# Performance work log

Hardware: AMD Instinct MI355X
Metric: run time of the kernel (lower is better)

## Reference

```python
import jax, jax.numpy as jnp
import numpy as np

B, S, H = 32, 256, 128
K, C, DSUB, O = 8, 4096, 16, 6  # PQ subspaces, ncentroids=4096, subvector dim, bits/symbol


def setup_inputs() -> dict:
    key = jax.random.key(0)
    ks = jax.random.split(key, 8)
    return {
        "z": jax.random.normal(ks[0], (B, S, 3), jnp.float32),
        "W1": jax.random.normal(ks[1], (3, H), jnp.float32) * 0.3,
        "b1": jax.random.normal(ks[2], (H,), jnp.float32) * 0.1,
        "W2": jax.random.normal(ks[3], (H, H), jnp.float32) * 0.1,
        "b2": jax.random.normal(ks[4], (H,), jnp.float32) * 0.1,
        "centroids": jax.random.normal(ks[5], (K, C, DSUB), jnp.float32),
        "W3": jax.random.normal(ks[6], (H, O), jnp.float32) * 0.1,
        "b3": jax.random.normal(ks[7], (O,), jnp.float32) * 0.1,
    }


def reference(z, W1, b1, W2, b2, centroids, W3, b3):
    # Small demapper MLP (layers 1-2, exact dense math)
    h1 = jax.nn.relu(z @ W1 + b1)            # [B,S,H]
    h2 = jax.nn.relu(h1 @ W2 + b2)           # [B,S,H] == layer3in
    N = B * S
    x = h2.reshape(N, K, DSUB)               # split rows into K PQ subvectors
    # Encode: nearest centroid per subspace (||x-c||^2 argmin; ||x||^2 is constant per row)
    dots = jnp.einsum("nkd,kcd->nkc", x, centroids)      # [N,K,C]
    c_norm = jnp.sum(centroids * centroids, axis=-1)      # [K,C]
    codes = jnp.argmin(c_norm[None, :, :] - 2.0 * dots, axis=-1)  # [N,K] int
    # LUT: precomputed centroid @ W3 per subspace
    W3r = W3.reshape(K, DSUB, O)
    lut = jnp.einsum("kcd,kdo->kco", centroids, W3r)      # [K,C,O]
    # Approximate matmul: sum of LUT entries selected by codes
    approx = jnp.sum(lut[jnp.arange(K)[None, :], codes], axis=1)  # [N,O]
    llr = (approx + b3).reshape(B, S * O)                 # [B, n]
    return llr
```

## Files before the change

### kernel.cpp

```cpp
#include <hip/hip_runtime.h>
#include <hip/hip_fp16.h>
#include <stdint.h>

#define NROWS 8192
#define HDIM  128
#define KSUB  8
#define NC    4096
#define DSUB  16
#define OUTD  6

#define FB_TAU 6e-5f
#define DOTSCALE (-2.0f / 4096.0f)

typedef _Float16 f16x8 __attribute__((ext_vector_type(8)));
typedef float    f32x4 __attribute__((ext_vector_type(4)));

#define XK_OFF 0u
#define CN_OFF 4194304u
#define B1_OFF 4325376u
#define PK_OFF 6422528u

__global__ __launch_bounds__(256) void prep_kernel(
    const float* __restrict__ z, const float* __restrict__ W1, const float* __restrict__ b1,
    const float* __restrict__ W2, const float* __restrict__ b2,
    const float* __restrict__ ce,
    float* __restrict__ xk, float* __restrict__ cnorm, f16x8* __restrict__ B1S)
{
    __shared__ float h1s[16 * HDIM];
    __shared__ float w2s[HDIM * 64];
    const int t = threadIdx.x;
    const int half = blockIdx.x >> 9;
    const int row0 = (blockIdx.x & 511) * 16;

    if (blockIdx.x < 512) {
        const int e = blockIdx.x * 256 + t;
        const int k    = e >> 14;
        const int tile = (e >> 6) & 255;
        const int lane = e & 63;
        const int col  = lane & 15;
        const int quad = lane >> 4;
        const int dims = (quad & 1) * 8;
        const int part = quad >> 1;
        const int n = tile * 16 + col;
        const float* cp = &ce[((size_t)k * NC + n) * DSUB + dims];
        f16x8 hi, lo;
        #pragma unroll
        for (int j = 0; j < 8; ++j) {
            const float s = cp[j] * 16.0f;
            const _Float16 h = (_Float16)s;
            hi[j] = h;
            lo[j] = (_Float16)(s - (float)h);
        }
        B1S[e] = part ? lo : hi;
    }

    if (blockIdx.x < (KSUB * NC) / 256) {
        const int g = blockIdx.x * 256 + t;
        const float4* cp = (const float4*)&ce[(size_t)g * DSUB];
        float nn = 0.f;
        #pragma unroll
        for (int q = 0; q < 4; ++q) {
            const float4 v = cp[q];
            nn = fmaf(v.x, v.x, nn); nn = fmaf(v.y, v.y, nn);
            nn = fmaf(v.z, v.z, nn); nn = fmaf(v.w, v.w, nn);
        }
        cnorm[g] = nn;
    }

    {
        const float4* g4 = (const float4*)W2;
        float4* s4 = (float4*)w2s;
        #pragma unroll
        for (int q = 0; q < 8; ++q) {
            const int idx = t + q * 256;
            const int k  = idx >> 4;
            const int cg = idx & 15;
            s4[k * 16 + cg] = g4[k * 32 + half * 16 + cg];
        }
    }

    #pragma unroll
    for (int e = 0; e < 8; ++e) {
        const int idx = e * 256 + t;
        const int r = idx >> 7, j = idx & 127;
        const int n = row0 + r;
        float acc = b1[j];
        acc = fmaf(z[n * 3 + 0], W1[0 * HDIM + j], acc);
        acc = fmaf(z[n * 3 + 1], W1[1 * HDIM + j], acc);
        acc = fmaf(z[n * 3 + 2], W1[2 * HDIM + j], acc);
        h1s[idx] = fmaxf(acc, 0.f);
    }
    __syncthreads();

    const int c2 = (t & 31) * 2;
    const int r2 = (t >> 5) * 2;
    float acc[2][2];
    acc[0][0] = acc[0][1] = acc[1][0] = acc[1][1] = 0.f;

    for (int k4 = 0; k4 < HDIM; k4 += 4) {
        float hh[2][4], ww[4][2];
        #pragma unroll
        for (int q = 0; q < 2; ++q) {
            const float4 v = *(const float4*)&h1s[(r2 + q) * HDIM + k4];
            hh[q][0] = v.x; hh[q][1] = v.y; hh[q][2] = v.z; hh[q][3] = v.w;
        }
        #pragma unroll
        for (int p = 0; p < 4; ++p) {
            const float2 v = *(const float2*)&w2s[(k4 + p) * 64 + c2];
            ww[p][0] = v.x; ww[p][1] = v.y;
        }
        #pragma unroll
        for (int q = 0; q < 2; ++q)
            #pragma unroll
            for (int p = 0; p < 4; ++p) {
                acc[q][0] = fmaf(hh[q][p], ww[p][0], acc[q][0]);
                acc[q][1] = fmaf(hh[q][p], ww[p][1], acc[q][1]);
            }
    }

    const int col0 = half * 64 + c2;
    const float2 bb = *(const float2*)&b2[col0];
    const int kk = col0 >> 4;
    const int dd = col0 & 15;
    #pragma unroll
    for (int q = 0; q < 2; ++q) {
        float2 o;
        o.x = fmaxf(acc[q][0] + bb.x, 0.f);
        o.y = fmaxf(acc[q][1] + bb.y, 0.f);
        *(float2*)&xk[((size_t)kk * NROWS + (row0 + r2 + q)) * DSUB + dd] = o;
    }
}

__global__ __launch_bounds__(256, 8) void argmin_kernel(
    const float* __restrict__ xk, const f16x8* __restrict__ B1S,
    const float* __restrict__ cnorm, unsigned long long* __restrict__ pk)
{
    __shared__ f16x8 cs[8 * 64];
    __shared__ float cnL[1024];
    const int t = threadIdx.x;
    const int lane = t & 63;
    const int wid  = t >> 6;
    const int k  = blockIdx.y;
    const int cz = blockIdx.z;
    const int rb = blockIdx.x * 4 + wid;
    const int col  = lane & 15;
    const int quad = lane >> 4;
    const int dims = (quad & 1) * 8;
    const int part = quad >> 1;

    {
        const float* cnp0 = &cnorm[k * NC + cz * 1024];
        #pragma unroll
        for (int q = 0; q < 4; ++q) cnL[t + q * 256] = cnp0[t + q * 256];
    }

    f16x8 A[2], A2[2];
    #pragma unroll
    for (int g = 0; g < 2; ++g) {
        const int row = rb * 32 + g * 16 + col;
        const float* xp = &xk[((size_t)k * NROWS + row) * DSUB + dims];
        f16x8 hi, lo;
        #pragma unroll
        for (int j = 0; j < 8; ++j) {
            const float s = xp[j] * 256.0f;
            const _Float16 h = (_Float16)s;
            hi[j] = h;
            lo[j] = (_Float16)(s - (float)h);
        }
        A[g]  = part ? lo : hi;
        A2[g] = part ? hi : lo;
    }

    float m1[2][4], m2[2][4];
    int   idx[2][4];
    #pragma unroll
    for (int g = 0; g < 2; ++g)
        #pragma unroll
        for (int j = 0; j < 4; ++j) { m1[g][j] = 1e30f; m2[g][j] = 1e30f; idx[g][j] = 0; }

    const f16x8* gp = &B1S[((size_t)k * 256 + cz * 64) * 64];

    for (int ch = 0; ch < 8; ++ch) {
        __syncthreads();
        {
            const uint4* g4 = (const uint4*)(gp + (size_t)ch * 512);
            uint4* s4 = (uint4*)cs;
            #pragma unroll
            for (int q = 0; q < 2; ++q) s4[t + q * 256] = g4[t + q * 256];
        }
        __syncthreads();

        #pragma unroll 2
        for (int tt = 0; tt < 8; ++tt) {
            const f16x8 b1 = cs[tt * 64 + lane];
            const float nrm = cnL[(ch * 8 + tt) * 16 + col];
            const f32x4 zz = {0.f, 0.f, 0.f, 0.f};
            f32x4 p0 = __builtin_amdgcn_mfma_f32_16x16x32_f16(A[0],  b1, zz, 0, 0, 0);
            p0       = __builtin_amdgcn_mfma_f32_16x16x32_f16(A2[0], b1, p0, 0, 0, 0);
            f32x4 p1 = __builtin_amdgcn_mfma_f32_16x16x32_f16(A[1],  b1, zz, 0, 0, 0);
            p1       = __builtin_amdgcn_mfma_f32_16x16x32_f16(A2[1], b1, p1, 0, 0, 0);
            const int c = ((cz * 64 + ch * 8 + tt) << 4) + col;
            #pragma unroll
            for (int j = 0; j < 4; ++j) {
                {
                    const float s = fmaf(p0[j], DOTSCALE, nrm);
                    const bool lt = s < m1[0][j];
                    m2[0][j] = __builtin_amdgcn_fmed3f(s, m1[0][j], m2[0][j]);
                    idx[0][j] = lt ? c : idx[0][j];
                    m1[0][j] = fminf(s, m1[0][j]);
                }
                {
                    const float s = fmaf(p1[j], DOTSCALE, nrm);
                    const bool lt = s < m1[1][j];
                    m2[1][j] = __builtin_amdgcn_fmed3f(s, m1[1][j], m2[1][j]);
                    idx[1][j] = lt ? c : idx[1][j];
                    m1[1][j] = fminf(s, m1[1][j]);
                }
            }
        }
    }

    #pragma unroll
    for (int off = 1; off < 16; off <<= 1) {
        #pragma unroll
        for (int g = 0; g < 2; ++g)
            #pragma unroll
            for (int j = 0; j < 4; ++j) {
                const float om1 = __shfl_xor(m1[g][j], off, 64);
                const float om2 = __shfl_xor(m2[g][j], off, 64);
                const int  oidx = __shfl_xor(idx[g][j], off, 64);
                const bool better = (om1 < m1[g][j]) ||
                                    (om1 == m1[g][j] && oidx < idx[g][j]);
                m2[g][j] = fminf(fminf(m2[g][j], om2), fmaxf(m1[g][j], om1));
                m1[g][j] = better ? om1 : m1[g][j];
                idx[g][j] = better ? oidx : idx[g][j];
            }
    }

    if (col == 0) {
        #pragma unroll
        for (int g = 0; g < 2; ++g)
            #pragma unroll
            for (int j = 0; j < 4; ++j) {
                const int row = rb * 32 + g * 16 + quad * 4 + j;
                unsigned u = __float_as_uint(m1[g][j]);
                u = (u & 0x80000000u) ? ~u : (u | 0x80000000u);
                const unsigned short dh =
                    __half_as_ushort(__float2half(m2[g][j] - m1[g][j]));
                pk[((size_t)cz * NROWS + row) * KSUB + k] =
                    ((unsigned long long)u << 32) |
                    ((unsigned)dh << 16) | (unsigned)idx[g][j];
            }
    }
}

__global__ __launch_bounds__(256) void finish_kernel(
    const float* __restrict__ xk, const float* __restrict__ ce,
    const float* __restrict__ cnorm, const unsigned long long* __restrict__ pk,
    const float* __restrict__ W3, const float* __restrict__ b3,
    float* __restrict__ out)
{
    __shared__ int codes_s[128];
    __shared__ int wl_s[128];
    __shared__ int wcnt;
    const int t = threadIdx.x;
    const int row0 = blockIdx.x * 16;
    if (t == 0) wcnt = 0;
    __syncthreads();

    if (t < 128) {
        const int row = row0 + (t >> 3);
        const int k = t & 7;
        unsigned long long p[4];
        #pragma unroll
        for (int s = 0; s < 4; ++s)
            p[s] = pk[((size_t)s * NROWS + row) * KSUB + k];
        unsigned long long w = p[0];
        #pragma unroll
        for (int s = 1; s < 4; ++s) w = p[s] < w ? p[s] : w;
        const unsigned uw = (unsigned)(w >> 32);
        const float m1w = __uint_as_float((uw & 0x80000000u) ? (uw ^ 0x80000000u) : ~uw);
        float m2g = m1w + (float)__ushort_as_half((unsigned short)((unsigned)w >> 16));
        #pragma unroll
        for (int s = 0; s < 4; ++s) {
            if (p[s] != w) {
                const unsigned us = (unsigned)(p[s] >> 32);
                m2g = fminf(m2g, __uint_as_float(
                    (us & 0x80000000u) ? (us ^ 0x80000000u) : ~us));
            }
        }
        codes_s[t] = (int)(w & 0xFFFFull);
        if (m2g - m1w < FB_TAU) {
            const int slot = atomicAdd(&wcnt, 1);
            wl_s[slot] = t;
        }
    }
    __syncthreads();

    {
        const int lane = t & 63;
        const int wid = t >> 6;
        const int nitems = wcnt;
        for (int i = wid; i < nitems; i += 4) {
            const int wg = wl_s[i];
            const int row = row0 + (wg >> 3), k = wg & 7;
            float xr[DSUB];
            {
                const float* xp = &xk[((size_t)k * NROWS + row) * DSUB];
                #pragma unroll
                for (int q = 0; q < DSUB; q += 4) {
                    const float4 v = *(const float4*)&xp[q];
                    xr[q + 0] = -2.f * v.x; xr[q + 1] = -2.f * v.y;
                    xr[q + 2] = -2.f * v.z; xr[q + 3] = -2.f * v.w;
                }
            }
            float bm = 1e30f; int bi = NC;
            for (int c = lane; c < NC; c += 64) {
                const float* cp = &ce[((size_t)k * NC + c) * DSUB];
                float s = cnorm[k * NC + c];
                #pragma unroll
                for (int d = 0; d < DSUB; ++d) s = fmaf(xr[d], cp[d], s);
                if (s < bm) { bm = s; bi = c; }
            }
            #pragma unroll
            for (int off = 1; off < 64; off <<= 1) {
                const float om = __shfl_xor(bm, off, 64);
                const int  oi = __shfl_xor(bi, off, 64);
                const bool better = (om < bm) || (om == bm && oi < bi);
                bm = better ? om : bm;
                bi = better ? oi : bi;
            }
            if (lane == 0) codes_s[wg] = bi;
        }
    }
    __syncthreads();

    if (t < 16 * OUTD) {
        const int nl = t / OUTD;
        const int o = t - nl * OUTD;
        const int n = row0 + nl;
        float acc = b3[o];
        #pragma unroll
        for (int k = 0; k < KSUB; ++k) {
            const int code = codes_s[nl * KSUB + k];
            const float* cp = &ce[((size_t)k * NC + code) * DSUB];
            const float* wp = &W3[(k * DSUB) * OUTD + o];
            #pragma unroll
            for (int d = 0; d < DSUB; ++d)
                acc = fmaf(cp[d], wp[d * OUTD], acc);
        }
        out[n * OUTD + o] = acc;
    }
}

extern "C" void kernel_launch(void* const* d_in, const int* in_sizes, int n_in,
                              void* d_out, int out_size, void* d_ws, size_t ws_size,
                              hipStream_t stream)
{
    const float* z  = (const float*)d_in[0];
    const float* W1 = (const float*)d_in[1];
    const float* b1 = (const float*)d_in[2];
    const float* W2 = (const float*)d_in[3];
    const float* b2 = (const float*)d_in[4];
    const float* ce = (const float*)d_in[5];
    const float* W3 = (const float*)d_in[6];
    const float* b3 = (const float*)d_in[7];

    char* ws = (char*)d_ws;
    float* xk    = (float*)(ws + XK_OFF);
    float* cnorm = (float*)(ws + CN_OFF);
    f16x8* B1S   = (f16x8*)(ws + B1_OFF);
    unsigned long long* pk = (unsigned long long*)(ws + PK_OFF);

    hipLaunchKernelGGL(prep_kernel, dim3(1024), dim3(256), 0, stream,
                       z, W1, b1, W2, b2, ce, xk, cnorm, B1S);
    hipLaunchKernelGGL(argmin_kernel, dim3(64, 8, 4), dim3(256), 0, stream,
                       xk, B1S, cnorm, pk);
    hipLaunchKernelGGL(finish_kernel, dim3(512), dim3(256), 0, stream,
                       xk, ce, cnorm, pk, W3, b3, (float*)d_out);
}
```

Measured before the change: 177.3 us.

## Switch argmin distance MFMA to 32x32x16 tiles with split hi/lo operands

Replaces the 16x16x32 f16 MFMA tiling in the argmin kernel with 32x32x16 MFMAs. Each wave now covers 32 rows by 32 centroids per step, with explicit hi/lo cross products (four MFMAs) instead of packing hi/lo into the K dimension. The centroid pre-packing layout in prep_kernel and the output row mapping change to match, and the shuffle reduction widens to 32 lanes. Per-thread state grows to 16 rows of min/second-min/index, so the launch-bounds occupancy hint drops from 8 to 4 blocks. This trades register pressure and lower occupancy for fewer, larger MFMA issues and less LDS traffic per product.

Result: slower. 196.3 us (+10.7%).

```diff
diff --git a/kernel.cpp b/kernel.cpp
--- a/kernel.cpp
+++ b/kernel.cpp
@@ -14,6 +14,7 @@
 
 typedef _Float16 f16x8 __attribute__((ext_vector_type(8)));
 typedef float    f32x4 __attribute__((ext_vector_type(4)));
+typedef float    f32x16 __attribute__((ext_vector_type(16)));
 
 #define XK_OFF 0u
 #define CN_OFF 4194304u
@@ -35,13 +36,11 @@
     if (blockIdx.x < 512) {
         const int e = blockIdx.x * 256 + t;
         const int k    = e >> 14;
-        const int tile = (e >> 6) & 255;
+        const int tile = (e >> 7) & 127;
+        const int part = (e >> 6) & 1;
         const int lane = e & 63;
-        const int col  = lane & 15;
-        const int quad = lane >> 4;
-        const int dims = (quad & 1) * 8;
-        const int part = quad >> 1;
-        const int n = tile * 16 + col;
+        const int n    = tile * 32 + (lane & 31);
+        const int dims = (lane >> 5) * 8;
         const float* cp = &ce[((size_t)k * NC + n) * DSUB + dims];
         f16x8 hi, lo;
         #pragma unroll
@@ -131,7 +130,7 @@
     }
 }
 
-__global__ __launch_bounds__(256, 8) void argmin_kernel(
+__global__ __launch_bounds__(256, 4) void argmin_kernel(
     const float* __restrict__ xk, const f16x8* __restrict__ B1S,
     const float* __restrict__ cnorm, unsigned long long* __restrict__ pk)
 {
@@ -143,10 +142,8 @@
     const int k  = blockIdx.y;
     const int cz = blockIdx.z;
     const int rb = blockIdx.x * 4 + wid;
-    const int col  = lane & 15;
-    const int quad = lane >> 4;
-    const int dims = (quad & 1) * 8;
-    const int part = quad >> 1;
+    const int col  = lane & 31;
+    const int half = lane >> 5;
 
     {
         const float* cnp0 = &cnorm[k * NC + cz * 1024];
@@ -154,31 +151,25 @@
         for (int q = 0; q < 4; ++q) cnL[t + q * 256] = cnp0[t + q * 256];
     }
 
-    f16x8 A[2], A2[2];
-    #pragma unroll
-    for (int g = 0; g < 2; ++g) {
-        const int row = rb * 32 + g * 16 + col;
-        const float* xp = &xk[((size_t)k * NROWS + row) * DSUB + dims];
-        f16x8 hi, lo;
+    f16x8 Ah, Al;
+    {
+        const int row = rb * 32 + col;
+        const float* xp = &xk[((size_t)k * NROWS + row) * DSUB + half * 8];
         #pragma unroll
         for (int j = 0; j < 8; ++j) {
             const float s = xp[j] * 256.0f;
             const _Float16 h = (_Float16)s;
-            hi[j] = h;
-            lo[j] = (_Float16)(s - (float)h);
-        }
-        A[g]  = part ? lo : hi;
-        A2[g] = part ? hi : lo;
-    }
-
-    float m1[2][4], m2[2][4];
-    int   idx[2][4];
+            Ah[j] = h;
+            Al[j] = (_Float16)(s - (float)h);
+        }
+    }
+
+    float m1[16], m2[16];
+    int   idx[16];
     #pragma unroll
-    for (int g = 0; g < 2; ++g)
-        #pragma unroll
-        for (int j = 0; j < 4; ++j) { m1[g][j] = 1e30f; m2[g][j] = 1e30f; idx[g][j] = 0; }
-
-    const f16x8* gp = &B1S[((size_t)k * 256 + cz * 64) * 64];
+    for (int r = 0; r < 16; ++r) { m1[r] = 1e30f; m2[r] = 1e30f; idx[r] = 0; }
+
+    const f16x8* gp = &B1S[((size_t)(k * 128 + cz * 32) * 2) * 64];
 
     for (int ch = 0; ch < 8; ++ch) {
         __syncthreads();
@@ -190,67 +181,55 @@
         }
         __syncthreads();
 
-        #pragma unroll 2
-        for (int tt = 0; tt < 8; ++tt) {
-            const f16x8 b1 = cs[tt * 64 + lane];
-            const float nrm = cnL[(ch * 8 + tt) * 16 + col];
-            const f32x4 zz = {0.f, 0.f, 0.f, 0.f};
-            f32x4 p0 = __builtin_amdgcn_mfma_f32_16x16x32_f16(A[0],  b1, zz, 0, 0, 0);
-            p0       = __builtin_amdgcn_mfma_f32_16x16x32_f16(A2[0], b1, p0, 0, 0, 0);
-            f32x4 p1 = __builtin_amdgcn_mfma_f32_16x16x32_f16(A[1],  b1, zz, 0, 0, 0);
-            p1       = __builtin_amdgcn_mfma_f32_16x16x32_f16(A2[1], b1, p1, 0, 0, 0);
-            const int c = ((cz * 64 + ch * 8 + tt) << 4) + col;
-            #pragma unroll
-            for (int j = 0; j < 4; ++j) {
-                {
-                    const float s = fmaf(p0[j], DOTSCALE, nrm);
-                    const bool lt = s < m1[0][j];
-                    m2[0][j] = __builtin_amdgcn_fmed3f(s, m1[0][j], m2[0][j]);
-                    idx[0][j] = lt ? c : idx[0][j];
-                    m1[0][j] = fminf(s, m1[0][j]);
-                }
-                {
-                    const float s = fmaf(p1[j], DOTSCALE, nrm);
-                    const bool lt = s < m1[1][j];
-                    m2[1][j] = __builtin_amdgcn_fmed3f(s, m1[1][j], m2[1][j]);
-                    idx[1][j] = lt ? c : idx[1][j];
-                    m1[1][j] = fminf(s, m1[1][j]);
-                }
+        #pragma unroll
+        for (int tt = 0; tt < 4; ++tt) {
+            const f16x8 bh = cs[(tt * 2 + 0) * 64 + lane];
+            const f16x8 bl = cs[(tt * 2 + 1) * 64 + lane];
+            const float nrm = cnL[(ch * 4 + tt) * 32 + col];
+            const f32x16 zz = {0.f};
+            f32x16 p = __builtin_amdgcn_mfma_f32_32x32x16_f16(Al, bh, zz, 0, 0, 0);
+            p        = __builtin_amdgcn_mfma_f32_32x32x16_f16(Ah, bl, p,  0, 0, 0);
+            p        = __builtin_amdgcn_mfma_f32_32x32x16_f16(Al, bl, p,  0, 0, 0);
+            p        = __builtin_amdgcn_mfma_f32_32x32x16_f16(Ah, bh, p,  0, 0, 0);
+            const int c = ((cz * 32 + ch * 4 + tt) << 5) + col;
+            #pragma unroll
+            for (int r = 0; r < 16; ++r) {
+                const float s = fmaf(p[r], DOTSCALE, nrm);
+                const bool lt = s < m1[r];
+                m2[r] = __builtin_amdgcn_fmed3f(s, m1[r], m2[r]);
+                idx[r] = lt ? c : idx[r];
+                m1[r] = fminf(s, m1[r]);
             }
         }
     }
 
     #pragma unroll
-    for (int off = 1; off < 16; off <<= 1) {
-        #pragma unroll
-        for (int g = 0; g < 2; ++g)
-            #pragma unroll
-            for (int j = 0; j < 4; ++j) {
-                const float om1 = __shfl_xor(m1[g][j], off, 64);
-                const float om2 = __shfl_xor(m2[g][j], off, 64);
-                const int  oidx = __shfl_xor(idx[g][j], off, 64);
-                const bool better = (om1 < m1[g][j]) ||
-                                    (om1 == m1[g][j] && oidx < idx[g][j]);
-                m2[g][j] = fminf(fminf(m2[g][j], om2), fmaxf(m1[g][j], om1));
-                m1[g][j] = better ? om1 : m1[g][j];
-                idx[g][j] = better ? oidx : idx[g][j];
-            }
+    for (int off = 1; off < 32; off <<= 1) {
+        #pragma unroll
+        for (int r = 0; r < 16; ++r) {
+            const float om1 = __shfl_xor(m1[r], off, 64);
+            const float om2 = __shfl_xor(m2[r], off, 64);
+            const int  oidx = __shfl_xor(idx[r], off, 64);
+            const bool better = (om1 < m1[r]) ||
+                                (om1 == m1[r] && oidx < idx[r]);
+            m2[r] = fminf(fminf(m2[r], om2), fmaxf(m1[r], om1));
+            m1[r] = better ? om1 : m1[r];
+            idx[r] = better ? oidx : idx[r];
+        }
     }
 
     if (col == 0) {
         #pragma unroll
-        for (int g = 0; g < 2; ++g)
-            #pragma unroll
-            for (int j = 0; j < 4; ++j) {
-                const int row = rb * 32 + g * 16 + quad * 4 + j;
-                unsigned u = __float_as_uint(m1[g][j]);
-                u = (u & 0x80000000u) ? ~u : (u | 0x80000000u);
-                const unsigned short dh =
-                    __half_as_ushort(__float2half(m2[g][j] - m1[g][j]));
-                pk[((size_t)cz * NROWS + row) * KSUB + k] =
-                    ((unsigned long long)u << 32) |
-                    ((unsigned)dh << 16) | (unsigned)idx[g][j];
-            }
+        for (int r = 0; r < 16; ++r) {
+            const int row = rb * 32 + (r & 3) + 8 * (r >> 2) + 4 * half;
+            unsigned u = __float_as_uint(m1[r]);
+            u = (u & 0x80000000u) ? ~u : (u | 0x80000000u);
+            const unsigned short dh =
+                __half_as_ushort(__float2half(m2[r] - m1[r]));
+            pk[((size_t)cz * NROWS + row) * KSUB + k] =
+                ((unsigned long long)u << 32) |
+                ((unsigned)dh << 16) | (unsigned)idx[r];
+        }
     }
 }
 
```
